# Optimization experiments

Measured on AMD Instinct MI355X. Metric: run time of the kernel, lower is better.

The kernel has to match this reference:

```python
import jax, jax.numpy as jnp
import numpy as np
import math

N, E, H, A = 50000, 800000, 128, 8
D = H // A


def setup_inputs() -> dict:
    key = jax.random.key(0)
    ks = jax.random.split(key, 12)
    q = jax.random.normal(ks[0], (N, H), dtype=jnp.float32)
    k = jax.random.normal(ks[1], (N, H), dtype=jnp.float32)
    v = jax.random.normal(ks[2], (N, H), dtype=jnp.float32)
    Wq = jax.random.normal(ks[3], (H, H), dtype=jnp.float32) * 0.05
    bq = jax.random.normal(ks[4], (H,), dtype=jnp.float32) * 0.05
    Wk = jax.random.normal(ks[5], (H, H), dtype=jnp.float32) * 0.05
    bk = jax.random.normal(ks[6], (H,), dtype=jnp.float32) * 0.05
    Wv = jax.random.normal(ks[7], (H, H), dtype=jnp.float32) * 0.05
    bv = jax.random.normal(ks[8], (H,), dtype=jnp.float32) * 0.05
    # Ensure every node id appears at least once in q_indices so that
    # q_indices.unique() == arange(N) and the output shape is static [N, H].
    tail = jax.random.randint(ks[9], (E - N,), 0, N)
    q_indices = jnp.concatenate([jnp.arange(N), tail]).astype(jnp.int32)
    k_indices = jax.random.randint(ks[10], (E,), 0, N).astype(jnp.int32)
    return {"q": q, "k": k, "v": v, "Wq": Wq, "bq": bq, "Wk": Wk, "bk": bk,
            "Wv": Wv, "bv": bv, "q_indices": q_indices, "k_indices": k_indices}


def reference(q, k, v, Wq, bq, Wk, bk, Wv, bv, q_indices, k_indices):
    n = q.shape[0]
    # Gather node features per edge (irregular access).
    qe = q[q_indices]            # [E, H]
    ke = k[k_indices]            # [E, H]
    ve = v[k_indices]            # [E, H]
    # Linear projections (torch Linear: x @ W.T + b), split heads -> [E, A, D].
    Q = (qe @ Wq.T + bq).reshape(-1, A, D)
    K = (ke @ Wk.T + bk).reshape(-1, A, D)
    V = (ve @ Wv.T + bv).reshape(-1, A, D)
    # Per-edge scaled dot-product scores: [E, A].
    scores = jnp.einsum('ead,ead->ea', Q, K) / math.sqrt(D)
    # Segment softmax over edges sharing the same destination node
    # (faithful to the original: plain exp, no max subtraction).
    ex = jnp.exp(scores)                                        # [E, A]
    denom = jax.ops.segment_sum(ex, q_indices, num_segments=n)  # [N, A]
    probs = ex / denom[q_indices]                               # [E, A]
    # Scatter-aggregate weighted values per destination node: [N, A, D].
    ctx = jax.ops.segment_sum(probs[:, :, None] * V, q_indices, num_segments=n)
    # Merge heads -> [N, H].
    return ctx.reshape(n, A * D)
```

## Files before the change

### kernel.cpp

```cpp
#include <hip/hip_runtime.h>
#include <hip/hip_bf16.h>

#define HDIM 128
#define LDS_STRIDE 136

typedef __attribute__((ext_vector_type(8))) short bf16x8;
typedef __attribute__((ext_vector_type(4))) float f32x4;

__device__ inline unsigned short f2bf(float f) {
    return __builtin_bit_cast(unsigned short, __float2bfloat16(f));
}

__global__ void init_kernel(int* __restrict__ p, int n2,
                            const float* __restrict__ Wq, const float* __restrict__ Wk,
                            const float* __restrict__ Wv, unsigned short* __restrict__ Wopt) {
    int i = blockIdx.x * 256 + threadIdx.x;
    if (i < n2) p[i] = 0;
    if (i < 3 * HDIM * HDIM) {
        int j  = i & 7;
        int l  = (i >> 3) & 63;
        int ks = (i >> 9) & 3;
        int nt = (i >> 11) & 7;
        int m  = i >> 14;
        const float* W = (m == 0) ? Wq : (m == 1) ? Wk : Wv;
        int row = nt * 16 + (l & 15);
        int col = ks * 32 + ((l >> 4) << 3) + j;
        Wopt[i] = f2bf(W[row * HDIM + col]);
    }
}

__global__ void proj_mfma(const float* __restrict__ qin, const float* __restrict__ kin,
                          const float* __restrict__ vin, const unsigned short* __restrict__ Wopt,
                          const float* __restrict__ bq, const float* __restrict__ bk,
                          const float* __restrict__ bv,
                          unsigned short* __restrict__ Qb, unsigned short* __restrict__ Kb,
                          unsigned short* __restrict__ Vb, int n)
{
    __shared__ unsigned short tile[64 * LDS_STRIDE];

    const int tid  = threadIdx.x;
    const int lane = tid & 63;
    const int wv   = tid >> 6;
    const int m    = blockIdx.y;
    const long node0 = (long)blockIdx.x * 64;

    const float* x = (m == 0) ? qin : (m == 1) ? kin : vin;
    const float* b = (m == 0) ? bq  : (m == 1) ? bk  : bv;
    unsigned short* O = (m == 0) ? Qb : (m == 1) ? Kb : Vb;
    const unsigned short* Wm = Wopt + (size_t)m * HDIM * HDIM;

    #pragma unroll
    for (int it = 0; it < 8; ++it) {
        int f   = it * 256 + tid;
        int row = f >> 5;
        int c4  = f & 31;
        long node = node0 + row;
        float4 val = make_float4(0.f, 0.f, 0.f, 0.f);
        if (node < n) val = ((const float4*)(x + node * HDIM))[c4];
        ushort4 h;
        h.x = f2bf(val.x); h.y = f2bf(val.y); h.z = f2bf(val.z); h.w = f2bf(val.w);
        *(ushort4*)&tile[row * LDS_STRIDE + c4 * 4] = h;
    }
    __syncthreads();

    const int r15  = lane & 15;
    const int quad = lane >> 4;

    bf16x8 af[4];
    #pragma unroll
    for (int ks = 0; ks < 4; ++ks)
        af[ks] = *(const bf16x8*)&tile[(wv * 16 + r15) * LDS_STRIDE + quad * 8 + ks * 32];

    f32x4 acc[8];
    #pragma unroll
    for (int nt = 0; nt < 8; ++nt) {
        acc[nt] = (f32x4){0.f, 0.f, 0.f, 0.f};
        #pragma unroll
        for (int ks = 0; ks < 4; ++ks) {
            const bf16x8 wfrag =
                *(const bf16x8*)(Wm + ((size_t)((nt * 4 + ks) * 64) + lane) * 8);
            acc[nt] = __builtin_amdgcn_mfma_f32_16x16x32_bf16(af[ks], wfrag, acc[nt], 0, 0, 0);
        }
    }
    __syncthreads();

    #pragma unroll
    for (int nt = 0; nt < 8; ++nt) {
        const int c = nt * 16 + r15;
        const float bias = b[c];
        #pragma unroll
        for (int r = 0; r < 4; ++r)
            tile[(wv * 16 + quad * 4 + r) * LDS_STRIDE + c] = f2bf(acc[nt][r] + bias);
    }
    __syncthreads();

    #pragma unroll
    for (int it = 0; it < 4; ++it) {
        int g   = it * 256 + tid;
        int row = g >> 4;
        int col = (g & 15) * 8;
        long node = node0 + row;
        if (node < n) {
            ushort4 lo = *(const ushort4*)&tile[row * LDS_STRIDE + col];
            ushort4 hi = *(const ushort4*)&tile[row * LDS_STRIDE + col + 4];
            uint4 out4;
            out4.x = (unsigned)lo.x | ((unsigned)lo.y << 16);
            out4.y = (unsigned)lo.z | ((unsigned)lo.w << 16);
            out4.z = (unsigned)hi.x | ((unsigned)hi.y << 16);
            out4.w = (unsigned)hi.z | ((unsigned)hi.w << 16);
            *(uint4*)&O[node * HDIM + col] = out4;
        }
    }
}

__global__ void deg_kernel(const int* __restrict__ qidx, int* __restrict__ deg, int E) {
    int e = blockIdx.x * blockDim.x + threadIdx.x;
    if (e < E) atomicAdd(&deg[qidx[e]], 1);
}

__global__ void scan_block(const int* __restrict__ deg, int* __restrict__ offs,
                           int* __restrict__ bsum, int n) {
    __shared__ int ws[17];
    const int tid = threadIdx.x;
    const int lane = tid & 63, wv = tid >> 6;
    int i = blockIdx.x * 1024 + tid;
    int v = (i < n) ? deg[i] : 0;
    int sc = v;
    #pragma unroll
    for (int d = 1; d < 64; d <<= 1) {
        int t = __shfl_up(sc, d, 64);
        if (lane >= d) sc += t;
    }
    if (lane == 63) ws[wv] = sc;
    __syncthreads();
    if (tid == 0) {
        int base = 0;
        #pragma unroll
        for (int w = 0; w < 16; ++w) { int t = ws[w]; ws[w] = base; base += t; }
        ws[16] = base;
    }
    __syncthreads();
    if (i < n) offs[i] = ws[wv] + (sc - v);
    if (tid == 0) bsum[blockIdx.x] = ws[16];
}

__global__ void scan_tops(int* __restrict__ bsum, int nb) {
    if (nb <= 64) {
        int lane = threadIdx.x;
        int v = (lane < nb) ? bsum[lane] : 0;
        int sc = v;
        #pragma unroll
        for (int d = 1; d < 64; d <<= 1) {
            int t = __shfl_up(sc, d, 64);
            if (lane >= d) sc += t;
        }
        if (lane < nb) bsum[lane] = sc - v;
    } else if (threadIdx.x == 0) {
        int base = 0;
        for (int i = 0; i < nb; ++i) { int t = bsum[i]; bsum[i] = base; base += t; }
    }
}

__global__ void scan_add(const int* __restrict__ bsum, int* __restrict__ offs,
                         int n, int E) {
    int i = blockIdx.x * blockDim.x + threadIdx.x;
    if (i < n) offs[i] += bsum[i >> 10];
    if (i == 0) offs[n] = E;
}

__global__ void fill_kernel(const int* __restrict__ qidx, const int* __restrict__ kidx,
                            const int* __restrict__ offs, int* __restrict__ cursor,
                            int* __restrict__ srcl, int E) {
    int e = blockIdx.x * blockDim.x + threadIdx.x;
    if (e < E) {
        int d = qidx[e];
        int pos = offs[d] + atomicAdd(&cursor[d], 1);
        srcl[pos] = kidx[e];
    }
}

__global__ void agg_kernel(const unsigned* __restrict__ Qu, const unsigned* __restrict__ Ku,
                           const unsigned* __restrict__ Vu,
                           const int* __restrict__ offs, const int* __restrict__ srcl,
                           float* __restrict__ out, int n)
{
    const int lane = threadIdx.x & 63;
    const int wid  = threadIdx.x >> 6;
    const int node = blockIdx.x * 4 + wid;
    if (node >= n) return;

    unsigned qu = Qu[(size_t)node * 64 + lane];
    const float qx = __uint_as_float(qu << 16);
    const float qy = __uint_as_float(qu & 0xffff0000u);

    float acc0 = 0.f, acc1 = 0.f, dsum = 0.f;
    const int beg = offs[node], end = offs[node + 1];

#define EDGE_STEP(ku, vu)                                                      \
    {                                                                          \
        float kx = __uint_as_float((ku) << 16);                                \
        float ky = __uint_as_float((ku) & 0xffff0000u);                        \
        float vx = __uint_as_float((vu) << 16);                                \
        float vy = __uint_as_float((vu) & 0xffff0000u);                        \
        float part = qx * kx + qy * ky;                                        \
        part += __shfl_xor(part, 1, 64);                                       \
        part += __shfl_xor(part, 2, 64);                                       \
        part += __shfl_xor(part, 4, 64);                                       \
        float w = __expf(part * 0.25f);                                        \
        dsum += w; acc0 += w * vx; acc1 += w * vy;                             \
    }

    for (int base = beg; base < end; base += 64) {
        int cnt = min(64, end - base);
        int my = (base + lane < end) ? srcl[base + lane] : 0;
        int j = 0;
        for (; j + 4 <= cnt; j += 4) {
            int s0 = __shfl(my, j,     64);
            int s1 = __shfl(my, j + 1, 64);
            int s2 = __shfl(my, j + 2, 64);
            int s3 = __shfl(my, j + 3, 64);
            unsigned k0 = Ku[(size_t)s0 * 64 + lane];
            unsigned v0 = Vu[(size_t)s0 * 64 + lane];
            unsigned k1 = Ku[(size_t)s1 * 64 + lane];
            unsigned v1 = Vu[(size_t)s1 * 64 + lane];
            unsigned k2 = Ku[(size_t)s2 * 64 + lane];
            unsigned v2 = Vu[(size_t)s2 * 64 + lane];
            unsigned k3 = Ku[(size_t)s3 * 64 + lane];
            unsigned v3 = Vu[(size_t)s3 * 64 + lane];
            EDGE_STEP(k0, v0); EDGE_STEP(k1, v1);
            EDGE_STEP(k2, v2); EDGE_STEP(k3, v3);
        }
        for (; j < cnt; ++j) {
            int s = __shfl(my, j, 64);
            unsigned kk = Ku[(size_t)s * 64 + lane];
            unsigned vv = Vu[(size_t)s * 64 + lane];
            EDGE_STEP(kk, vv);
        }
    }
#undef EDGE_STEP

    float inv = 1.f / dsum;
    *(float2*)&out[(size_t)node * HDIM + lane * 2] = make_float2(acc0 * inv, acc1 * inv);
}

extern "C" void kernel_launch(void* const* d_in, const int* in_sizes, int n_in,
                              void* d_out, int out_size, void* d_ws, size_t ws_size,
                              hipStream_t stream) {
    const float* q  = (const float*)d_in[0];
    const float* k  = (const float*)d_in[1];
    const float* v  = (const float*)d_in[2];
    const float* Wq = (const float*)d_in[3];
    const float* bq = (const float*)d_in[4];
    const float* Wk = (const float*)d_in[5];
    const float* bk = (const float*)d_in[6];
    const float* Wv = (const float*)d_in[7];
    const float* bv = (const float*)d_in[8];
    const int* qidx = (const int*)d_in[9];
    const int* kidx = (const int*)d_in[10];
    float* out = (float*)d_out;

    const int N = in_sizes[0] / HDIM;
    const int E = in_sizes[9];

    char* p = (char*)d_ws;
    unsigned short* Qb = (unsigned short*)p; p += (size_t)N * HDIM * sizeof(unsigned short);
    unsigned short* Kb = (unsigned short*)p; p += (size_t)N * HDIM * sizeof(unsigned short);
    unsigned short* Vb = (unsigned short*)p; p += (size_t)N * HDIM * sizeof(unsigned short);
    unsigned short* Wopt = (unsigned short*)p; p += (size_t)3 * HDIM * HDIM * sizeof(unsigned short);
    int* deg    = (int*)p; p += (size_t)N * sizeof(int);
    int* cursor = (int*)p; p += (size_t)N * sizeof(int);
    int* offs   = (int*)p; p += (size_t)(N + 1) * sizeof(int);
    int* bsum   = (int*)p; p += 64 * sizeof(int);
    int* srcl   = (int*)p; p += (size_t)E * sizeof(int);

    const int nb = (N + 1023) / 1024;
    const int initn = (2 * N > 3 * HDIM * HDIM) ? 2 * N : 3 * HDIM * HDIM;

    init_kernel<<<(initn + 255) / 256, 256, 0, stream>>>(deg, 2 * N, Wq, Wk, Wv, Wopt);
    {
        dim3 grid((N + 63) / 64, 3);
        proj_mfma<<<grid, 256, 0, stream>>>(q, k, v, Wopt, bq, bk, bv, Qb, Kb, Vb, N);
    }
    deg_kernel<<<(E + 255) / 256, 256, 0, stream>>>(qidx, deg, E);
    scan_block<<<nb, 1024, 0, stream>>>(deg, offs, bsum, N);
    scan_tops<<<1, 64, 0, stream>>>(bsum, nb);
    scan_add<<<(N + 1023) / 1024, 1024, 0, stream>>>(bsum, offs, N, E);
    fill_kernel<<<(E + 255) / 256, 256, 0, stream>>>(qidx, kidx, offs, cursor, srcl, E);
    agg_kernel<<<(N + 3) / 4, 256, 0, stream>>>((const unsigned*)Qb, (const unsigned*)Kb,
                                                (const unsigned*)Vb, offs, srcl, out, N);
}
```

Measured before the change: 281.9 us.

## Fuse degree counting into projection, merge scan kernels, record ranks, half-wave aggregation

Degree counting moves into the projection launch as an extra grid row, and each edge's atomic return value is saved as its rank. The fill kernel then places edges without a second atomic pass, and the cursor buffer goes away. The two scan-tail kernels merge into one that scans the block sums per block. The aggregation kernel assigns 32 lanes per node with 8-byte loads, so each wave handles two nodes. This cuts launch count and atomic traffic, at the cost of an extra rank array of size E and a per-block redundant top-level scan.

```diff
diff --git a/kernel.cpp b/kernel.cpp
--- a/kernel.cpp
+++ b/kernel.cpp
@@ -10,12 +10,14 @@
 __device__ inline unsigned short f2bf(float f) {
     return __builtin_bit_cast(unsigned short, __float2bfloat16(f));
 }
-
-__global__ void init_kernel(int* __restrict__ p, int n2,
+__device__ inline float bflo(unsigned u) { return __uint_as_float(u << 16); }
+__device__ inline float bfhi(unsigned u) { return __uint_as_float(u & 0xffff0000u); }
+
+__global__ void init_kernel(int* __restrict__ deg, int n,
                             const float* __restrict__ Wq, const float* __restrict__ Wk,
                             const float* __restrict__ Wv, unsigned short* __restrict__ Wopt) {
     int i = blockIdx.x * 256 + threadIdx.x;
-    if (i < n2) p[i] = 0;
+    if (i < n) deg[i] = 0;
     if (i < 3 * HDIM * HDIM) {
         int j  = i & 7;
         int l  = (i >> 3) & 63;
@@ -29,14 +31,23 @@
     }
 }
 
-__global__ void proj_mfma(const float* __restrict__ qin, const float* __restrict__ kin,
-                          const float* __restrict__ vin, const unsigned short* __restrict__ Wopt,
-                          const float* __restrict__ bq, const float* __restrict__ bk,
-                          const float* __restrict__ bv,
-                          unsigned short* __restrict__ Qb, unsigned short* __restrict__ Kb,
-                          unsigned short* __restrict__ Vb, int n)
+__global__ void proj_deg(const float* __restrict__ qin, const float* __restrict__ kin,
+                         const float* __restrict__ vin, const unsigned short* __restrict__ Wopt,
+                         const float* __restrict__ bq, const float* __restrict__ bk,
+                         const float* __restrict__ bv,
+                         unsigned short* __restrict__ Qb, unsigned short* __restrict__ Kb,
+                         unsigned short* __restrict__ Vb,
+                         const int* __restrict__ qidx, int* __restrict__ deg,
+                         int* __restrict__ rank, int E, int n, int nbx)
 {
     __shared__ unsigned short tile[64 * LDS_STRIDE];
+
+    if (blockIdx.y == 3) {
+        int e = blockIdx.x * 256 + threadIdx.x;
+        if (e < E) rank[e] = atomicAdd(&deg[qidx[e]], 1);
+        return;
+    }
+    if (blockIdx.x >= (unsigned)nbx) return;
 
     const int tid  = threadIdx.x;
     const int lane = tid & 63;
@@ -113,11 +124,6 @@
     }
 }
 
-__global__ void deg_kernel(const int* __restrict__ qidx, int* __restrict__ deg, int E) {
-    int e = blockIdx.x * blockDim.x + threadIdx.x;
-    if (e < E) atomicAdd(&deg[qidx[e]], 1);
-}
-
 __global__ void scan_block(const int* __restrict__ deg, int* __restrict__ offs,
                            int* __restrict__ bsum, int n) {
     __shared__ int ws[17];
@@ -144,103 +150,87 @@
     if (tid == 0) bsum[blockIdx.x] = ws[16];
 }
 
-__global__ void scan_tops(int* __restrict__ bsum, int nb) {
-    if (nb <= 64) {
-        int lane = threadIdx.x;
-        int v = (lane < nb) ? bsum[lane] : 0;
+__global__ void scan_addtops(const int* __restrict__ bsum, int* __restrict__ offs,
+                             int n, int E, int nb) {
+    __shared__ int s_base;
+    const int tid = threadIdx.x;
+    if (tid < 64) {
+        int v = (tid < nb) ? bsum[tid] : 0;
         int sc = v;
         #pragma unroll
         for (int d = 1; d < 64; d <<= 1) {
             int t = __shfl_up(sc, d, 64);
-            if (lane >= d) sc += t;
-        }
-        if (lane < nb) bsum[lane] = sc - v;
-    } else if (threadIdx.x == 0) {
-        int base = 0;
-        for (int i = 0; i < nb; ++i) { int t = bsum[i]; bsum[i] = base; base += t; }
-    }
-}
-
-__global__ void scan_add(const int* __restrict__ bsum, int* __restrict__ offs,
-                         int n, int E) {
-    int i = blockIdx.x * blockDim.x + threadIdx.x;
-    if (i < n) offs[i] += bsum[i >> 10];
-    if (i == 0) offs[n] = E;
+            if (tid >= d) sc += t;
+        }
+        if (tid == blockIdx.x) s_base = sc - v;
+    }
+    __syncthreads();
+    int i = blockIdx.x * 1024 + tid;
+    if (i < n) offs[i] += s_base;
+    if (blockIdx.x == 0 && tid == 0) offs[n] = E;
 }
 
 __global__ void fill_kernel(const int* __restrict__ qidx, const int* __restrict__ kidx,
-                            const int* __restrict__ offs, int* __restrict__ cursor,
+                            const int* __restrict__ offs, const int* __restrict__ rank,
                             int* __restrict__ srcl, int E) {
     int e = blockIdx.x * blockDim.x + threadIdx.x;
-    if (e < E) {
-        int d = qidx[e];
-        int pos = offs[d] + atomicAdd(&cursor[d], 1);
-        srcl[pos] = kidx[e];
-    }
-}
-
-__global__ void agg_kernel(const unsigned* __restrict__ Qu, const unsigned* __restrict__ Ku,
-                           const unsigned* __restrict__ Vu,
+    if (e < E) srcl[offs[qidx[e]] + rank[e]] = kidx[e];
+}
+
+__global__ void agg_kernel(const uint2* __restrict__ Q2, const uint2* __restrict__ K2,
+                           const uint2* __restrict__ V2,
                            const int* __restrict__ offs, const int* __restrict__ srcl,
                            float* __restrict__ out, int n)
 {
-    const int lane = threadIdx.x & 63;
-    const int wid  = threadIdx.x >> 6;
-    const int node = blockIdx.x * 4 + wid;
+    const int tid  = threadIdx.x;
+    const int l32  = tid & 31;
+    const int node = blockIdx.x * 8 + (tid >> 5);
     if (node >= n) return;
 
-    unsigned qu = Qu[(size_t)node * 64 + lane];
-    const float qx = __uint_as_float(qu << 16);
-    const float qy = __uint_as_float(qu & 0xffff0000u);
-
-    float acc0 = 0.f, acc1 = 0.f, dsum = 0.f;
+    const uint2 qp = Q2[(size_t)node * 32 + l32];
+    const float qx = bflo(qp.x), qy = bfhi(qp.x), qz = bflo(qp.y), qw = bfhi(qp.y);
+
+    float dsum = 0.f, a0 = 0.f, a1 = 0.f, a2 = 0.f, a3 = 0.f;
     const int beg = offs[node], end = offs[node + 1];
-
-#define EDGE_STEP(ku, vu)                                                      \
+    const int srcbase = tid & 32;
+
+#define EDGE_STEP(kp, vp)                                                      \
     {                                                                          \
-        float kx = __uint_as_float((ku) << 16);                                \
-        float ky = __uint_as_float((ku) & 0xffff0000u);                        \
-        float vx = __uint_as_float((vu) << 16);                                \
-        float vy = __uint_as_float((vu) & 0xffff0000u);                        \
-        float part = qx * kx + qy * ky;                                        \
+        float part = qx * bflo((kp).x) + qy * bfhi((kp).x)                     \
+                   + qz * bflo((kp).y) + qw * bfhi((kp).y);                    \
         part += __shfl_xor(part, 1, 64);                                       \
         part += __shfl_xor(part, 2, 64);                                       \
-        part += __shfl_xor(part, 4, 64);                                       \
         float w = __expf(part * 0.25f);                                        \
-        dsum += w; acc0 += w * vx; acc1 += w * vy;                             \
-    }
-
-    for (int base = beg; base < end; base += 64) {
-        int cnt = min(64, end - base);
-        int my = (base + lane < end) ? srcl[base + lane] : 0;
+        dsum += w;                                                             \
+        a0 += w * bflo((vp).x); a1 += w * bfhi((vp).x);                        \
+        a2 += w * bflo((vp).y); a3 += w * bfhi((vp).y);                        \
+    }
+
+    for (int base = beg; base < end; base += 32) {
+        int cnt = min(32, end - base);
+        int my = (base + l32 < end) ? srcl[base + l32] : 0;
         int j = 0;
-        for (; j + 4 <= cnt; j += 4) {
-            int s0 = __shfl(my, j,     64);
-            int s1 = __shfl(my, j + 1, 64);
-            int s2 = __shfl(my, j + 2, 64);
-            int s3 = __shfl(my, j + 3, 64);
-            unsigned k0 = Ku[(size_t)s0 * 64 + lane];
-            unsigned v0 = Vu[(size_t)s0 * 64 + lane];
-            unsigned k1 = Ku[(size_t)s1 * 64 + lane];
-            unsigned v1 = Vu[(size_t)s1 * 64 + lane];
-            unsigned k2 = Ku[(size_t)s2 * 64 + lane];
-            unsigned v2 = Vu[(size_t)s2 * 64 + lane];
-            unsigned k3 = Ku[(size_t)s3 * 64 + lane];
-            unsigned v3 = Vu[(size_t)s3 * 64 + lane];
+        for (; j + 2 <= cnt; j += 2) {
+            int s0 = __shfl(my, srcbase + j,     64);
+            int s1 = __shfl(my, srcbase + j + 1, 64);
+            uint2 k0 = K2[(size_t)s0 * 32 + l32];
+            uint2 v0 = V2[(size_t)s0 * 32 + l32];
+            uint2 k1 = K2[(size_t)s1 * 32 + l32];
+            uint2 v1 = V2[(size_t)s1 * 32 + l32];
             EDGE_STEP(k0, v0); EDGE_STEP(k1, v1);
-            EDGE_STEP(k2, v2); EDGE_STEP(k3, v3);
         }
         for (; j < cnt; ++j) {
-            int s = __shfl(my, j, 64);
-            unsigned kk = Ku[(size_t)s * 64 + lane];
-            unsigned vv = Vu[(size_t)s * 64 + lane];
+            int s = __shfl(my, srcbase + j, 64);
+            uint2 kk = K2[(size_t)s * 32 + l32];
+            uint2 vv = V2[(size_t)s * 32 + l32];
             EDGE_STEP(kk, vv);
         }
     }
 #undef EDGE_STEP
 
     float inv = 1.f / dsum;
-    *(float2*)&out[(size_t)node * HDIM + lane * 2] = make_float2(acc0 * inv, acc1 * inv);
+    float4 r = make_float4(a0 * inv, a1 * inv, a2 * inv, a3 * inv);
+    *(float4*)&out[(size_t)node * HDIM + l32 * 4] = r;
 }
 
 extern "C" void kernel_launch(void* const* d_in, const int* in_sizes, int n_in,
@@ -267,25 +257,26 @@
     unsigned short* Kb = (unsigned short*)p; p += (size_t)N * HDIM * sizeof(unsigned short);
     unsigned short* Vb = (unsigned short*)p; p += (size_t)N * HDIM * sizeof(unsigned short);
     unsigned short* Wopt = (unsigned short*)p; p += (size_t)3 * HDIM * HDIM * sizeof(unsigned short);
-    int* deg    = (int*)p; p += (size_t)N * sizeof(int);
-    int* cursor = (int*)p; p += (size_t)N * sizeof(int);
-    int* offs   = (int*)p; p += (size_t)(N + 1) * sizeof(int);
-    int* bsum   = (int*)p; p += 64 * sizeof(int);
-    int* srcl   = (int*)p; p += (size_t)E * sizeof(int);
-
-    const int nb = (N + 1023) / 1024;
-    const int initn = (2 * N > 3 * HDIM * HDIM) ? 2 * N : 3 * HDIM * HDIM;
-
-    init_kernel<<<(initn + 255) / 256, 256, 0, stream>>>(deg, 2 * N, Wq, Wk, Wv, Wopt);
+    int* deg  = (int*)p; p += (size_t)N * sizeof(int);
+    int* offs = (int*)p; p += (size_t)(N + 1) * sizeof(int);
+    int* bsum = (int*)p; p += 64 * sizeof(int);
+    int* rank = (int*)p; p += (size_t)E * sizeof(int);
+    int* srcl = (int*)p; p += (size_t)E * sizeof(int);
+
+    const int nbx = (N + 63) / 64;
+    const int neb = (E + 255) / 256;
+    const int nb  = (N + 1023) / 1024;
+    const int initn = (N > 3 * HDIM * HDIM) ? N : 3 * HDIM * HDIM;
+
+    init_kernel<<<(initn + 255) / 256, 256, 0, stream>>>(deg, N, Wq, Wk, Wv, Wopt);
     {
-        dim3 grid((N + 63) / 64, 3);
-        proj_mfma<<<grid, 256, 0, stream>>>(q, k, v, Wopt, bq, bk, bv, Qb, Kb, Vb, N);
-    }
-    deg_kernel<<<(E + 255) / 256, 256, 0, stream>>>(qidx, deg, E);
+        dim3 grid((nbx > neb) ? nbx : neb, 4);
+        proj_deg<<<grid, 256, 0, stream>>>(q, k, v, Wopt, bq, bk, bv, Qb, Kb, Vb,
+                                           qidx, deg, rank, E, N, nbx);
+    }
     scan_block<<<nb, 1024, 0, stream>>>(deg, offs, bsum, N);
-    scan_tops<<<1, 64, 0, stream>>>(bsum, nb);
-    scan_add<<<(N + 1023) / 1024, 1024, 0, stream>>>(bsum, offs, N, E);
-    fill_kernel<<<(E + 255) / 256, 256, 0, stream>>>(qidx, kidx, offs, cursor, srcl, E);
-    agg_kernel<<<(N + 3) / 4, 256, 0, stream>>>((const unsigned*)Qb, (const unsigned*)Kb,
-                                                (const unsigned*)Vb, offs, srcl, out, N);
-}
+    scan_addtops<<<nb, 1024, 0, stream>>>(bsum, offs, N, E, nb);
+    fill_kernel<<<neb, 256, 0, stream>>>(qidx, kidx, offs, rank, srcl, E);
+    agg_kernel<<<(N + 7) / 8, 256, 0, stream>>>((const uint2*)Qb, (const uint2*)Kb,
+                                                (const uint2*)Vb, offs, srcl, out, N);
+}
```

Measured after the change: 248.4 us. -11.9%, faster.
